# Kernel optimization log

Hardware: AMD Instinct MI355X
Metric: run time of the kernel (lower is better)

## Reference

```python
import jax, jax.numpy as jnp
import numpy as np

N = 50000
E = 1600000
SI, SO, VI, VO, H, SVOD = 128, 128, 16, 16, 16, 3
EPS = 1e-8


def _safe_norm(x, axis, keepdims=False):
    return jnp.sqrt(jnp.sum(x * x, axis=axis, keepdims=keepdims) + EPS)


def setup_inputs() -> dict:
    key = jax.random.key(0)
    ks = jax.random.split(key, 13)

    def lin(k, fan_in, shape):
        b = 1.0 / np.sqrt(fan_in)
        return jax.random.uniform(k, shape, jnp.float32, -b, b)

    merged_dim = H + SI + 3 * SVOD  # 153
    return {
        "s": jax.random.normal(ks[0], (N, SI), jnp.float32),
        "v": jax.random.normal(ks[1], (N, VI, 3), jnp.float32),
        "frames": jax.random.normal(ks[2], (E, 3, 3), jnp.float32),
        "W_vd": lin(ks[3], VI, (VI, H)),            # vector_down (no bias)
        "W_vdf": lin(ks[4], VI, (VI, SVOD)),        # vector_down_frames (no bias)
        "W_so": lin(ks[5], merged_dim, (merged_dim, SO)),  # scalar_out
        "b_so": lin(ks[6], merged_dim, (SO,)),
        "W_vu": lin(ks[7], H, (H, VO)),             # vector_up (no bias)
        "W_vosf": lin(ks[8], SO, (SO, 3 * SVOD)),   # vector_out_scale_frames
        "b_vosf": lin(ks[9], SO, (3 * SVOD,)),
        "W_vuf": lin(ks[10], SVOD, (SVOD, VO)),     # vector_up_frames (no bias)
        "edge_index": jax.random.randint(ks[11], (2, E), 0, N, jnp.int32),
        "node_inputs": 1,
    }


def reference(s, v, frames, W_vd, W_vdf, W_so, b_so, W_vu, W_vosf, b_vosf, W_vuf, edge_index, node_inputs):
    # node_inputs is assumed truthy (node-wise GCP): gather by source node, scatter-mean back.
    row = edge_index[0]
    deg = jax.ops.segment_sum(jnp.ones((E,), s.dtype), row, num_segments=N)
    inv_deg = 1.0 / jnp.maximum(deg, 1.0)

    v_pre = jnp.swapaxes(v, -1, -2)                 # [N, 3, VI]
    vh = v_pre @ W_vd                                # [N, 3, H]
    vnorm = _safe_norm(vh, axis=-2)                  # [N, H]
    vdf = v_pre @ W_vdf                              # [N, 3, SVOD]

    # scalarize: project gathered source-node vectors onto per-edge frames, scatter-mean
    local = jnp.einsum('eij,ejc->eic', frames, vdf[row])       # [E, 3, SVOD]
    local9 = jnp.swapaxes(local, -1, -2).reshape(E, 3 * SVOD)  # [E, 9]
    sh = jax.ops.segment_sum(local9, row, num_segments=N) * inv_deg[:, None]  # [N, 9]

    merged = jnp.concatenate([s, vnorm, sh], axis=-1)          # [N, SI+H+9]
    scalar_rep = merged @ W_so + b_so                           # [N, SO]

    # vector path with frame gate
    vr = jnp.swapaxes(vh @ W_vu, -1, -2)                        # [N, VO, 3]
    gate = jax.nn.sigmoid(scalar_rep) @ W_vosf + b_vosf         # [N, 9]
    # vectorize: expand gate scalars back into vectors via frames, scatter-mean
    g = gate[row].reshape(E, 3, 3)
    gv_e = jnp.einsum('eji,ejk->eik', g, frames)                # [E, 3, 3]
    gv = jax.ops.segment_sum(gv_e, row, num_segments=N) * inv_deg[:, None, None]  # [N, 3, 3]
    gvr = jnp.swapaxes(jnp.swapaxes(gv, -1, -2) @ W_vuf, -1, -2)  # [N, VO, 3]
    vr = vr * jax.nn.sigmoid(_safe_norm(gvr, axis=-1, keepdims=True))

    return jax.nn.relu(scalar_rep), vr
```

## Files before the change

kernel.cpp:

```cpp
#include <hip/hip_runtime.h>

#define N_NODES 50000
#define N_EDGES 1600000
#define NPB     16
#define NCHAIN  16
#define KSTR    168
#define EPSV    1e-8f

typedef float f32x4 __attribute__((ext_vector_type(4)));
typedef short s16x8 __attribute__((ext_vector_type(8)));

struct f4u { float a, b, c, d; };

__device__ __forceinline__ float sigmoidf_(float x) { return 1.0f / (1.0f + __expf(-x)); }
__device__ __forceinline__ short f2bf(float x) {
    unsigned u = __float_as_uint(x);
    unsigned r = (u + 0x7FFFu + ((u >> 16) & 1u)) >> 16;
    return (short)r;
}
__device__ __forceinline__ float bf2f(short h) {
    return __uint_as_float(((unsigned)(unsigned short)h) << 16);
}
__device__ __forceinline__ unsigned pkbf(float lo, float hi) {
    return (unsigned)(unsigned short)f2bf(lo) | ((unsigned)(unsigned short)f2bf(hi) << 16);
}
__device__ __forceinline__ float bflo(unsigned u) { return __uint_as_float(u << 16); }
__device__ __forceinline__ float bfhi(unsigned u) { return __uint_as_float(u & 0xffff0000u); }

__global__ __launch_bounds__(256) void init_kernel(
    const float* __restrict__ W_so, short* __restrict__ WThi, short* __restrict__ WTlo,
    int* __restrict__ head) {
    int i = blockIdx.x * 256 + threadIdx.x;
    if (i < 128 * 160) {
        int o = i / 160, k = i - o * 160;
        float w = (k < 153) ? W_so[k * 128 + o] : 0.0f;
        short hh = f2bf(w);
        WThi[i] = hh;
        WTlo[i] = f2bf(w - bf2f(hh));
    }
    if (i < N_NODES * NCHAIN) head[i] = -1;
}

__global__ __launch_bounds__(256) void bucket_fat_kernel(
    const int* __restrict__ row,
    const float* __restrict__ frames,
    int* __restrict__ head,
    unsigned* __restrict__ pay) {
    int e = blockIdx.x * 256 + threadIdx.x;
    if (e >= N_EDGES) return;
    int r = row[e];
    int prev = atomicExch(&head[r * NCHAIN + (e & (NCHAIN - 1))], e);
    const float* f = frames + (size_t)e * 9;
    f4u x = ((const f4u*)f)[0];
    f4u y = ((const f4u*)f)[1];
    float z8 = f[8];
    uint4* dst = (uint4*)(pay + (size_t)e * 8);
    dst[0] = make_uint4(pkbf(x.a, x.b), pkbf(x.c, x.d), pkbf(y.a, y.b), pkbf(y.c, y.d));
    dst[1] = make_uint4((unsigned)(unsigned short)f2bf(z8), (unsigned)prev, 0u, 0u);
}

__global__ __launch_bounds__(256) void bucket_thin_kernel(
    const int* __restrict__ row,
    int* __restrict__ head,
    int* __restrict__ nxt) {
    int e = blockIdx.x * 256 + threadIdx.x;
    if (e >= N_EDGES) return;
    int r = row[e];
    int prev = atomicExch(&head[r * NCHAIN + (e & (NCHAIN - 1))], e);
    nxt[e] = prev;
}

template<int MODE>
__global__ __launch_bounds__(256) void node_kernel(
    const float* __restrict__ s,
    const float* __restrict__ v,
    const unsigned* __restrict__ pay,
    const float* __restrict__ frames,
    const float* __restrict__ W_vd,
    const float* __restrict__ W_vdf,
    const short* __restrict__ WThi,
    const short* __restrict__ WTlo,
    const float* __restrict__ b_so,
    const float* __restrict__ W_vu,
    const float* __restrict__ W_vosf,
    const float* __restrict__ b_vosf,
    const float* __restrict__ W_vuf,
    const int* __restrict__ head,
    const int* __restrict__ nxt,
    float* __restrict__ out0,
    float* __restrict__ out1)
{
    __shared__ __align__(16) short AL[2][NPB][KSTR];
    __shared__ float vL[NPB][48];
    __shared__ float vhL[NPB][3][16];
    __shared__ float FbarL[NPB][9];
    __shared__ float gateL[NPB][12];

    float (*sigL)[128] = (float (*)[128])&AL[0][0][0];

    const int t = threadIdx.x;
    const int base = blockIdx.x * NPB;
    const int nn = t >> 4, h = t & 15;
    const int n = base + nn;

    int e = head[(size_t)n * NCHAIN + h];

#pragma unroll
    for (int r = 0; r < 3; r++) vL[nn][h * 3 + r] = v[(size_t)n * 48 + h * 3 + r];
    {
        const float4* sp4 = (const float4*)(s + (size_t)n * 128 + h * 8);
        float4 s0 = sp4[0], s1 = sp4[1];
        float sv[8] = {s0.x, s0.y, s0.z, s0.w, s1.x, s1.y, s1.z, s1.w};
        s16x8 shi, slo;
#pragma unroll
        for (int j = 0; j < 8; j++) {
            short hh = f2bf(sv[j]);
            shi[j] = hh;
            slo[j] = f2bf(sv[j] - bf2f(hh));
        }
        *(s16x8*)&AL[0][nn][h * 8] = shi;
        *(s16x8*)&AL[1][nn][h * 8] = slo;
    }

    float fs[10];
#pragma unroll
    for (int k = 0; k < 10; k++) fs[k] = 0.f;
    float invdeg;
    {
        if (MODE == 1) {
            while (e >= 0) {
                const uint4* p = (const uint4*)(pay + (size_t)e * 8);
                uint4 b = p[1];
                uint4 a = p[0];
                int en = (int)b.y;
                fs[0] += bflo(a.x); fs[1] += bfhi(a.x);
                fs[2] += bflo(a.y); fs[3] += bfhi(a.y);
                fs[4] += bflo(a.z); fs[5] += bfhi(a.z);
                fs[6] += bflo(a.w); fs[7] += bfhi(a.w);
                fs[8] += bflo(b.x);
                fs[9] += 1.0f;
                e = en;
            }
        } else {
            while (e >= 0) {
                int en = nxt[e];
                const float* f = frames + (size_t)e * 9;
                f4u x = ((const f4u*)f)[0];
                f4u y = ((const f4u*)f)[1];
                float z8 = f[8];
                fs[0] += x.a; fs[1] += x.b; fs[2] += x.c; fs[3] += x.d;
                fs[4] += y.a; fs[5] += y.b; fs[6] += y.c; fs[7] += y.d;
                fs[8] += z8;
                fs[9] += 1.0f;
                e = en;
            }
        }
#pragma unroll
        for (int m = 1; m < 16; m <<= 1) {
#pragma unroll
            for (int k = 0; k < 10; k++) fs[k] += __shfl_xor(fs[k], m);
        }
        invdeg = 1.0f / fmaxf(fs[9], 1.0f);
        if (h < 9) FbarL[nn][h] = fs[h] * invdeg;
    }
    __syncthreads();

    {
        float vh0 = 0.f, vh1 = 0.f, vh2 = 0.f;
#pragma unroll
        for (int i = 0; i < 16; i++) {
            float w = W_vd[i * 16 + h];
            vh0 += vL[nn][i * 3 + 0] * w;
            vh1 += vL[nn][i * 3 + 1] * w;
            vh2 += vL[nn][i * 3 + 2] * w;
        }
        vhL[nn][0][h] = vh0; vhL[nn][1][h] = vh1; vhL[nn][2][h] = vh2;
        float vn = sqrtf(vh0 * vh0 + vh1 * vh1 + vh2 * vh2 + EPSV);
        short hh = f2bf(vn);
        AL[0][nn][128 + h] = hh;
        AL[1][nn][128 + h] = f2bf(vn - bf2f(hh));
        if (h < 9) {
            const int c = h / 3, i = h % 3;
            float a = 0.f;
#pragma unroll
            for (int j = 0; j < 3; j++) {
                float vd = 0.f;
#pragma unroll
                for (int ii = 0; ii < 16; ii++) vd += vL[nn][ii * 3 + j] * W_vdf[ii * 3 + c];
                a += (fs[i * 3 + j] * invdeg) * vd;
            }
            short hs = f2bf(a);
            AL[0][nn][144 + h] = hs;
            AL[1][nn][144 + h] = f2bf(a - bf2f(hs));
        } else {
            AL[0][nn][144 + h] = 0;
            AL[1][nn][144 + h] = 0;
        }
    }
    __syncthreads();

    {
        const int w = t >> 6;
        const int lane = t & 63;
        const int quad = lane >> 4;
        const int col = lane & 15;
        const int o0 = w * 32 + col, o1 = o0 + 16;
        f32x4 acc0 = (f32x4){0.f, 0.f, 0.f, 0.f};
        f32x4 acc1 = (f32x4){0.f, 0.f, 0.f, 0.f};
#pragma unroll
        for (int kk = 0; kk < 5; kk++) {
            const int krow = kk * 32 + quad * 8;
            s16x8 ahi = *(const s16x8*)&AL[0][col][krow];
            s16x8 alo = *(const s16x8*)&AL[1][col][krow];
            s16x8 b0h = *(const s16x8*)&WThi[o0 * 160 + krow];
            s16x8 b0l = *(const s16x8*)&WTlo[o0 * 160 + krow];
            s16x8 b1h = *(const s16x8*)&WThi[o1 * 160 + krow];
            s16x8 b1l = *(const s16x8*)&WTlo[o1 * 160 + krow];
            acc0 = __builtin_amdgcn_mfma_f32_16x16x32_bf16(ahi, b0h, acc0, 0, 0, 0);
            acc0 = __builtin_amdgcn_mfma_f32_16x16x32_bf16(ahi, b0l, acc0, 0, 0, 0);
            acc0 = __builtin_amdgcn_mfma_f32_16x16x32_bf16(alo, b0h, acc0, 0, 0, 0);
            acc1 = __builtin_amdgcn_mfma_f32_16x16x32_bf16(ahi, b1h, acc1, 0, 0, 0);
            acc1 = __builtin_amdgcn_mfma_f32_16x16x32_bf16(ahi, b1l, acc1, 0, 0, 0);
            acc1 = __builtin_amdgcn_mfma_f32_16x16x32_bf16(alo, b1h, acc1, 0, 0, 0);
        }
        __syncthreads();
        {
            float b0 = b_so[o0], b1 = b_so[o1];
#pragma unroll
            for (int r = 0; r < 4; r++) {
                int nl = quad * 4 + r;
                float v0 = acc0[r] + b0;
                float v1 = acc1[r] + b1;
                out0[(size_t)(base + nl) * 128 + o0] = fmaxf(v0, 0.0f);
                out0[(size_t)(base + nl) * 128 + o1] = fmaxf(v1, 0.0f);
                sigL[nl][o0] = sigmoidf_(v0);
                sigL[nl][o1] = sigmoidf_(v1);
            }
        }
    }
    __syncthreads();

    {
        const float* sp = &sigL[nn][h * 8];
        float4 s0 = *(const float4*)sp;
        float4 s1 = *(const float4*)(sp + 4);
        float sv[8] = {s0.x, s0.y, s0.z, s0.w, s1.x, s1.y, s1.z, s1.w};
        float p[9];
#pragma unroll
        for (int k = 0; k < 9; k++) p[k] = 0.f;
#pragma unroll
        for (int i = 0; i < 8; i++) {
            int o = h * 8 + i;
#pragma unroll
            for (int k = 0; k < 9; k++) p[k] += sv[i] * W_vosf[o * 9 + k];
        }
#pragma unroll
        for (int m = 1; m < 16; m <<= 1) {
#pragma unroll
            for (int k = 0; k < 9; k++) p[k] += __shfl_xor(p[k], m);
        }
        if (h < 9) gateL[nn][h] = p[h] + b_vosf[h];
    }
    __syncthreads();

    {
        int o = h;
        float gv[9];
#pragma unroll
        for (int i = 0; i < 3; i++)
#pragma unroll
            for (int kk = 0; kk < 3; kk++) {
                float a = 0.f;
#pragma unroll
                for (int j = 0; j < 3; j++) a += gateL[nn][j * 3 + i] * FbarL[nn][j * 3 + kk];
                gv[i * 3 + kk] = a;
            }
        float gvr[3];
#pragma unroll
        for (int kk = 0; kk < 3; kk++) {
            float a = 0.f;
#pragma unroll
            for (int i = 0; i < 3; i++) a += gv[i * 3 + kk] * W_vuf[i * 16 + o];
            gvr[kk] = a;
        }
        float gn2 = sqrtf(gvr[0] * gvr[0] + gvr[1] * gvr[1] + gvr[2] * gvr[2] + EPSV);
        float sg = sigmoidf_(gn2);
#pragma unroll
        for (int c = 0; c < 3; c++) {
            float a = 0.f;
#pragma unroll
            for (int h2 = 0; h2 < 16; h2++) a += vhL[nn][c][h2] * W_vu[h2 * 16 + o];
            out1[(size_t)n * 48 + o * 3 + c] = a * sg;
        }
    }
}

extern "C" void kernel_launch(void* const* d_in, const int* in_sizes, int n_in,
                              void* d_out, int out_size, void* d_ws, size_t ws_size,
                              hipStream_t stream) {
    const float* s      = (const float*)d_in[0];
    const float* v      = (const float*)d_in[1];
    const float* frames = (const float*)d_in[2];
    const float* W_vd   = (const float*)d_in[3];
    const float* W_vdf  = (const float*)d_in[4];
    const float* W_so   = (const float*)d_in[5];
    const float* b_so   = (const float*)d_in[6];
    const float* W_vu   = (const float*)d_in[7];
    const float* W_vosf = (const float*)d_in[8];
    const float* b_vosf = (const float*)d_in[9];
    const float* W_vuf  = (const float*)d_in[10];
    const int* edge_index = (const int*)d_in[11];

    const size_t head_b = (size_t)N_NODES * NCHAIN * sizeof(int);
    const size_t wt_b   = (size_t)128 * 160 * sizeof(short);
    const size_t pay_off = head_b + 2 * wt_b;
    int*   head = (int*)d_ws;
    short* WThi = (short*)((char*)d_ws + head_b);
    short* WTlo = WThi + 128 * 160;
    float* out0 = (float*)d_out;
    float* out1 = out0 + (size_t)N_NODES * 128;

    const size_t fat_need = pay_off + (size_t)N_EDGES * 32;
    init_kernel<<<(N_NODES * NCHAIN + 255) / 256, 256, 0, stream>>>(W_so, WThi, WTlo, head);

    if (ws_size >= fat_need) {
        unsigned* pay = (unsigned*)((char*)d_ws + pay_off);
        bucket_fat_kernel<<<(N_EDGES + 255) / 256, 256, 0, stream>>>(edge_index, frames, head, pay);
        node_kernel<1><<<N_NODES / NPB, 256, 0, stream>>>(
            s, v, pay, frames, W_vd, W_vdf, WThi, WTlo, b_so, W_vu, W_vosf, b_vosf, W_vuf,
            head, (const int*)nullptr, out0, out1);
    } else {
        int* nxt = (int*)((char*)d_ws + pay_off);
        bucket_thin_kernel<<<(N_EDGES + 255) / 256, 256, 0, stream>>>(edge_index, head, nxt);
        node_kernel<0><<<N_NODES / NPB, 256, 0, stream>>>(
            s, v, (const unsigned*)nullptr, frames, W_vd, W_vdf, WThi, WTlo, b_so, W_vu, W_vosf, b_vosf, W_vuf,
            head, nxt, out0, out1);
    }
}
```

Measured before the change: 268.0 us.

## Bucket edges into fixed-capacity per-node slot arrays with linked-list overflow

Replaces the per-node linked-list chains with a capped slot array. Each edge atomically takes a slot in one of 8 per-node sub-buckets and writes its packed bf16 frame payload there; edges beyond the cap fall back to a linked list. The node kernel then reads contiguous slots without the serial pointer chase, and gets the degree directly from the counter. It also swaps the head init kernel for memsets and adds a workspace-size-dependent path selection. The cost is a larger workspace and a possible overflow tail when degree exceeds the cap.

After: 290.0 us. +8.2%, slower.

```diff
diff --git a/kernel.cpp b/kernel.cpp
--- a/kernel.cpp
+++ b/kernel.cpp
@@ -3,6 +3,7 @@
 #define N_NODES 50000
 #define N_EDGES 1600000
 #define NPB     16
+#define NCH     8
 #define NCHAIN  16
 #define KSTR    168
 #define EPSV    1e-8f
@@ -27,18 +28,42 @@
 __device__ __forceinline__ float bflo(unsigned u) { return __uint_as_float(u << 16); }
 __device__ __forceinline__ float bfhi(unsigned u) { return __uint_as_float(u & 0xffff0000u); }
 
-__global__ __launch_bounds__(256) void init_kernel(
-    const float* __restrict__ W_so, short* __restrict__ WThi, short* __restrict__ WTlo,
-    int* __restrict__ head) {
+__global__ __launch_bounds__(256) void wsplit_kernel(
+    const float* __restrict__ W_so, short* __restrict__ WThi, short* __restrict__ WTlo) {
     int i = blockIdx.x * 256 + threadIdx.x;
-    if (i < 128 * 160) {
-        int o = i / 160, k = i - o * 160;
-        float w = (k < 153) ? W_so[k * 128 + o] : 0.0f;
-        short hh = f2bf(w);
-        WThi[i] = hh;
-        WTlo[i] = f2bf(w - bf2f(hh));
-    }
-    if (i < N_NODES * NCHAIN) head[i] = -1;
+    if (i >= 128 * 160) return;
+    int o = i / 160, k = i - o * 160;
+    float w = (k < 153) ? W_so[k * 128 + o] : 0.0f;
+    short hh = f2bf(w);
+    WThi[i] = hh;
+    WTlo[i] = f2bf(w - bf2f(hh));
+}
+
+__global__ __launch_bounds__(256) void bucket_csr8i_kernel(
+    const int* __restrict__ row,
+    const float* __restrict__ frames,
+    int* __restrict__ cnt,
+    int* __restrict__ head2,
+    int* __restrict__ nxt,
+    unsigned* __restrict__ pay,
+    int cap) {
+    int e = blockIdx.x * 256 + threadIdx.x;
+    if (e >= N_EDGES) return;
+    int r = row[e];
+    int c = e & (NCH - 1);
+    int slot = atomicAdd(&cnt[r * NCH + c], 1);
+    if (slot < cap) {
+        const float* f = frames + (size_t)e * 9;
+        f4u x = ((const f4u*)f)[0];
+        f4u y = ((const f4u*)f)[1];
+        float z8 = f[8];
+        unsigned* dst = pay + (((size_t)r * cap + slot) * NCH + c) * 8;
+        ((uint4*)dst)[0] = make_uint4(pkbf(x.a, x.b), pkbf(x.c, x.d), pkbf(y.a, y.b), pkbf(y.c, y.d));
+        ((uint4*)dst)[1] = make_uint4((unsigned)(unsigned short)f2bf(z8), 0u, 0u, 0u);
+    } else {
+        int prev = atomicExch(&head2[r * NCH + c], e);
+        nxt[e] = prev;
+    }
 }
 
 __global__ __launch_bounds__(256) void bucket_fat_kernel(
@@ -85,8 +110,10 @@
     const float* __restrict__ W_vosf,
     const float* __restrict__ b_vosf,
     const float* __restrict__ W_vuf,
-    const int* __restrict__ head,
+    const int* __restrict__ cnt_or_head,
+    const int* __restrict__ head2,
     const int* __restrict__ nxt,
+    int cap,
     float* __restrict__ out0,
     float* __restrict__ out1)
 {
@@ -103,7 +130,9 @@
     const int nn = t >> 4, h = t & 15;
     const int n = base + nn;
 
-    int e = head[(size_t)n * NCHAIN + h];
+    int e0;
+    if (MODE == 2) e0 = cnt_or_head[n * NCH + (h & (NCH - 1))];
+    else           e0 = cnt_or_head[(size_t)n * NCHAIN + h];
 
 #pragma unroll
     for (int r = 0; r < 3; r++) vL[nn][h * 3 + r] = v[(size_t)n * 48 + h * 3 + r];
@@ -127,7 +156,38 @@
     for (int k = 0; k < 10; k++) fs[k] = 0.f;
     float invdeg;
     {
-        if (MODE == 1) {
+        if (MODE == 2) {
+            const int cn = e0;
+            const int lim = cn < cap ? cn : cap;
+            for (int sl = (h >> 3); sl < lim; sl += 2) {
+                const unsigned* p = pay + (((size_t)n * cap + sl) * NCH + (h & (NCH - 1))) * 8;
+                uint4 a = *(const uint4*)p;
+                unsigned b = p[4];
+                fs[0] += bflo(a.x); fs[1] += bfhi(a.x);
+                fs[2] += bflo(a.y); fs[3] += bfhi(a.y);
+                fs[4] += bflo(a.z); fs[5] += bfhi(a.z);
+                fs[6] += bflo(a.w); fs[7] += bfhi(a.w);
+                fs[8] += bflo(b);
+            }
+            if (h < NCH) {
+                fs[9] = (float)cn;
+                if (cn > cap) {
+                    int e2 = head2[n * NCH + h];
+                    while (e2 >= 0) {
+                        int en = nxt[e2];
+                        const float* f = frames + (size_t)e2 * 9;
+                        f4u x = ((const f4u*)f)[0];
+                        f4u y = ((const f4u*)f)[1];
+                        float z8 = f[8];
+                        fs[0] += x.a; fs[1] += x.b; fs[2] += x.c; fs[3] += x.d;
+                        fs[4] += y.a; fs[5] += y.b; fs[6] += y.c; fs[7] += y.d;
+                        fs[8] += z8;
+                        e2 = en;
+                    }
+                }
+            }
+        } else if (MODE == 1) {
+            int e = e0;
             while (e >= 0) {
                 const uint4* p = (const uint4*)(pay + (size_t)e * 8);
                 uint4 b = p[1];
@@ -142,6 +202,7 @@
                 e = en;
             }
         } else {
+            int e = e0;
             while (e >= 0) {
                 int en = nxt[e];
                 const float* f = frames + (size_t)e * 9;
@@ -311,29 +372,61 @@
     const float* W_vuf  = (const float*)d_in[10];
     const int* edge_index = (const int*)d_in[11];
 
-    const size_t head_b = (size_t)N_NODES * NCHAIN * sizeof(int);
-    const size_t wt_b   = (size_t)128 * 160 * sizeof(short);
-    const size_t pay_off = head_b + 2 * wt_b;
-    int*   head = (int*)d_ws;
-    short* WThi = (short*)((char*)d_ws + head_b);
-    short* WTlo = WThi + 128 * 160;
     float* out0 = (float*)d_out;
     float* out1 = out0 + (size_t)N_NODES * 128;
 
-    const size_t fat_need = pay_off + (size_t)N_EDGES * 32;
-    init_kernel<<<(N_NODES * NCHAIN + 255) / 256, 256, 0, stream>>>(W_so, WThi, WTlo, head);
-
-    if (ws_size >= fat_need) {
-        unsigned* pay = (unsigned*)((char*)d_ws + pay_off);
-        bucket_fat_kernel<<<(N_EDGES + 255) / 256, 256, 0, stream>>>(edge_index, frames, head, pay);
+    const size_t wt_b = (size_t)128 * 160 * sizeof(short);
+    const size_t cnt_b   = (size_t)N_NODES * NCH * sizeof(int);
+    const size_t head2_b = (size_t)N_NODES * NCH * sizeof(int);
+    const size_t nxt_b   = (size_t)N_EDGES * sizeof(int);
+    const size_t csr_base = cnt_b + head2_b + 2 * wt_b + nxt_b;
+    long cap = 0;
+    if (ws_size > csr_base)
+        cap = (long)((ws_size - csr_base) / ((size_t)N_NODES * NCH * 32));
+    if (cap > 16) cap = 16;
+
+    const size_t head_b  = (size_t)N_NODES * NCHAIN * sizeof(int);
+    const size_t fat_off = head_b + 2 * wt_b;
+    const size_t fat_need = fat_off + (size_t)N_EDGES * 32;
+
+    if (cap >= 6) {
+        int*      cnt   = (int*)d_ws;
+        int*      head2 = (int*)((char*)d_ws + cnt_b);
+        short*    WThi  = (short*)((char*)d_ws + cnt_b + head2_b);
+        short*    WTlo  = WThi + 128 * 160;
+        int*      nxt   = (int*)((char*)d_ws + cnt_b + head2_b + 2 * wt_b);
+        unsigned* pay   = (unsigned*)((char*)d_ws + csr_base);
+        hipMemsetAsync(cnt, 0x00, cnt_b, stream);
+        hipMemsetAsync(head2, 0xFF, head2_b, stream);
+        wsplit_kernel<<<(128 * 160 + 255) / 256, 256, 0, stream>>>(W_so, WThi, WTlo);
+        bucket_csr8i_kernel<<<(N_EDGES + 255) / 256, 256, 0, stream>>>(
+            edge_index, frames, cnt, head2, nxt, pay, (int)cap);
+        node_kernel<2><<<N_NODES / NPB, 256, 0, stream>>>(
+            s, v, pay, frames, W_vd, W_vdf, WThi, WTlo, b_so, W_vu, W_vosf, b_vosf, W_vuf,
+            cnt, head2, nxt, (int)cap, out0, out1);
+    } else if (ws_size >= fat_need) {
+        int*      head = (int*)d_ws;
+        short*    WThi = (short*)((char*)d_ws + head_b);
+        short*    WTlo = WThi + 128 * 160;
+        unsigned* pay  = (unsigned*)((char*)d_ws + fat_off);
+        hipMemsetAsync(head, 0xFF, head_b, stream);
+        wsplit_kernel<<<(128 * 160 + 255) / 256, 256, 0, stream>>>(W_so, WThi, WTlo);
+        bucket_fat_kernel<<<(N_EDGES + 255) / 256, 256, 0, stream>>>(
+            edge_index, frames, head, pay);
         node_kernel<1><<<N_NODES / NPB, 256, 0, stream>>>(
             s, v, pay, frames, W_vd, W_vdf, WThi, WTlo, b_so, W_vu, W_vosf, b_vosf, W_vuf,
-            head, (const int*)nullptr, out0, out1);
+            head, (const int*)nullptr, (const int*)nullptr, 0, out0, out1);
     } else {
-        int* nxt = (int*)((char*)d_ws + pay_off);
-        bucket_thin_kernel<<<(N_EDGES + 255) / 256, 256, 0, stream>>>(edge_index, head, nxt);
+        int*   head = (int*)d_ws;
+        short* WThi = (short*)((char*)d_ws + head_b);
+        short* WTlo = WThi + 128 * 160;
+        int*   nxt  = (int*)((char*)d_ws + fat_off);
+        hipMemsetAsync(head, 0xFF, head_b, stream);
+        wsplit_kernel<<<(128 * 160 + 255) / 256, 256, 0, stream>>>(W_so, WThi, WTlo);
+        bucket_thin_kernel<<<(N_EDGES + 255) / 256, 256, 0, stream>>>(
+            edge_index, head, nxt);
         node_kernel<0><<<N_NODES / NPB, 256, 0, stream>>>(
-            s, v, (const unsigned*)nullptr, frames, W_vd, W_vdf, WThi, WTlo, b_so, W_vu, W_vosf, b_vosf, W_vuf,
-            head, nxt, out0, out1);
-    }
-}
+            s, v, (const unsigned*)nullptr, frames, W_vd, W_vdf, WThi, WTlo, b_so,
+            W_vu, W_vosf, b_vosf, W_vuf, head, (const int*)nullptr, nxt, 0, out0, out1);
+    }
+}
```
